# Kernel tuning notes

Hardware: AMD Instinct MI355X
Metric: run time of the kernel (lower is better)

## Reference

```python
import jax, jax.numpy as jnp
import numpy as np

N = 50000        # nodes
DEG = 16         # in-degree per node
E = N * DEG      # edges
NF = 32          # node_feats
H = 4            # heads
EF = 32          # e_feats
SLOPE = 0.2      # negative_slope


def setup_inputs() -> dict:
    key = jax.random.key(0)
    ks = jax.random.split(key, 8)
    h = jax.random.normal(ks[0], (N, NF), dtype=jnp.float32)
    e = jax.random.normal(ks[1], (E, EF), dtype=jnp.float32)
    src = jax.random.randint(ks[2], (E,), 0, N)
    # every node has exactly DEG incoming edges (sorted by dst)
    dst = jnp.repeat(jnp.arange(N), DEG)
    W_node = jax.random.normal(ks[3], (NF, H * NF), dtype=jnp.float32) * 0.1
    W_edge = jax.random.normal(ks[4], (EF, H * NF), dtype=jnp.float32) * 0.1
    w_att = jax.random.normal(ks[5], (H, 3 * NF), dtype=jnp.float32) * 0.1
    W_scale = jax.random.normal(ks[6], (H * NF, NF), dtype=jnp.float32) * 0.1
    bias = jnp.zeros((NF,), dtype=jnp.float32)
    return {"h": h, "e": e, "src": src, "dst": dst, "W_node": W_node,
            "W_edge": W_edge, "w_att": w_att, "W_scale": W_scale, "bias": bias}


def reference(h, e, src, dst, W_node, W_edge, w_att, W_scale, bias):
    wv = (h @ W_node).reshape(N, H, NF)       # [N,H,F]
    we = (e @ W_edge).reshape(E, H, NF)       # [E,H,F]
    u = wv[src]                               # [E,H,F] src features per edge
    v = wv[dst]                               # [E,H,F] dst features per edge
    # attention = leaky_relu(<concat(u,e,v), w_att>) without materializing concat
    wa_u, wa_e, wa_v = jnp.split(w_att, 3, axis=-1)  # each [H,F]
    attn = (jnp.einsum('ehf,hf->eh', u, wa_u)
            + jnp.einsum('ehf,hf->eh', we, wa_e)
            + jnp.einsum('ehf,hf->eh', v, wa_v))
    attn = jax.nn.leaky_relu(attn, SLOPE)     # [E,H]
    # segment softmax over incoming edges of each dst node (stable)
    m = jax.lax.stop_gradient(jax.ops.segment_max(attn, dst, num_segments=N))
    ex = jnp.exp(attn - m[dst])
    denom = jax.ops.segment_sum(ex, dst, num_segments=N)
    score = ex / denom[dst]                   # [E,H]
    msg = score[:, :, None] * u * we          # [E,H,F]
    agg = jax.ops.segment_sum(msg, dst, num_segments=N).reshape(N, H * NF)
    return agg @ W_scale + bias               # [N,F]
```

## Files before the change

kernel.cpp:

```cpp
#include <hip/hip_runtime.h>
#include <math.h>

#define N_NODES 50000
#define DEG 16
#define NF 32
#define NHEAD 4
#define HF (NHEAD * NF)
#define EF 32
#define SLOPE 0.2f

__device__ __forceinline__ float bcastf(float v, int srclane) {
    return __uint_as_float((unsigned)__builtin_amdgcn_readlane((int)__float_as_uint(v), srclane));
}

__global__ __launch_bounds__(256) void k1_wv(
    const float* __restrict__ hfeat,
    const float* __restrict__ W_node,
    const float* __restrict__ w_att,
    float* __restrict__ wv,
    float* __restrict__ att_src,
    float* __restrict__ att_dst)
{
    const int wave = threadIdx.x >> 6;
    const int lane = threadIdx.x & 63;
    const int n = blockIdx.x * 4 + wave;
    const int j0 = 2 * lane;
    const int hh = lane >> 4;
    const int f0 = j0 & 31;

    float hv = hfeat[n * NF + (lane & 31)];
    float acc0 = 0.f, acc1 = 0.f;
#pragma unroll
    for (int k = 0; k < NF; ++k) {
        float hk = bcastf(hv, k);
        float2 wk = *reinterpret_cast<const float2*>(&W_node[k * HF + j0]);
        acc0 = fmaf(hk, wk.x, acc0);
        acc1 = fmaf(hk, wk.y, acc1);
    }
    *reinterpret_cast<float2*>(&wv[(size_t)n * HF + j0]) = make_float2(acc0, acc1);

    float2 wau = *reinterpret_cast<const float2*>(&w_att[hh * (3 * NF) + f0]);
    float2 wav = *reinterpret_cast<const float2*>(&w_att[hh * (3 * NF) + 2 * NF + f0]);
    float du = acc0 * wau.x + acc1 * wau.y;
    float dv = acc0 * wav.x + acc1 * wav.y;
#pragma unroll
    for (int m = 1; m < 16; m <<= 1) {
        du += __shfl_xor(du, m, 64);
        dv += __shfl_xor(dv, m, 64);
    }
    if ((lane & 15) == 0) {
        att_src[n * NHEAD + hh] = du;
        att_dst[n * NHEAD + hh] = dv;
    }
}

__global__ __launch_bounds__(256) void k2_main(
    const float* __restrict__ efeat,
    const int*   __restrict__ src,
    const float* __restrict__ W_edge,
    const float* __restrict__ w_att,
    const float* __restrict__ W_scale,
    const float* __restrict__ bias,
    const float* __restrict__ wv,
    const float* __restrict__ att_src,
    const float* __restrict__ att_dst,
    float* __restrict__ out)
{
    __shared__ float lds_agg[4][HF];

    const int wave = threadIdx.x >> 6;
    const int lane = threadIdx.x & 63;
    const int n = blockIdx.x * 4 + wave;
    const int j0 = 2 * lane;
    const int hh = lane >> 4;
    const int f0 = j0 & 31;

    float2 W[EF];
#pragma unroll
    for (int k = 0; k < EF; ++k)
        W[k] = *reinterpret_cast<const float2*>(&W_edge[k * HF + j0]);

    const float* eblk = efeat + (size_t)n * DEG * EF;
    float4 ea = *reinterpret_cast<const float4*>(eblk + lane * 8);
    float4 eb4 = *reinterpret_cast<const float4*>(eblk + lane * 8 + 4);
    float ebf[8] = {ea.x, ea.y, ea.z, ea.w, eb4.x, eb4.y, eb4.z, eb4.w};

    int sv = src[n * DEG + (lane & 15)];

    float2 wae = *reinterpret_cast<const float2*>(&w_att[hh * (3 * NF) + NF + f0]);
    float dvv = att_dst[n * NHEAD + hh];

    float m = -INFINITY, l = 0.f, acc0 = 0.f, acc1 = 0.f;

#pragma unroll
    for (int ed = 0; ed < DEG; ++ed) {
        const int s = __builtin_amdgcn_readlane(sv, ed);
        float2 uu = *reinterpret_cast<const float2*>(&wv[(size_t)s * HF + j0]);

        float we0 = 0.f, we1 = 0.f;
#pragma unroll
        for (int k = 0; k < EF; ++k) {
            const int idx = ed * EF + k;
            float ek = bcastf(ebf[idx & 7], idx >> 3);
            we0 = fmaf(ek, W[k].x, we0);
            we1 = fmaf(ek, W[k].y, we1);
        }
        float ap = we0 * wae.x + we1 * wae.y;
        ap += __shfl_xor(ap, 1, 64);
        ap += __shfl_xor(ap, 2, 64);
        ap += __shfl_xor(ap, 4, 64);
        ap += __shfl_xor(ap, 8, 64);
        float a = ap + att_src[(size_t)s * NHEAD + hh] + dvv;
        a = (a > 0.f) ? a : a * SLOPE;

        float mn = fmaxf(m, a);
        float corr = __expf(m - mn);
        float ex = __expf(a - mn);
        l = l * corr + ex;
        acc0 = acc0 * corr + ex * (uu.x * we0);
        acc1 = acc1 * corr + ex * (uu.y * we1);
        m = mn;
    }
    const float inv = 1.f / l;
    lds_agg[wave][j0] = acc0 * inv;
    lds_agg[wave][j0 + 1] = acc1 * inv;
    __syncthreads();

    const int c = lane & 31;
    const int half = lane >> 5;
    float part = 0.f;
#pragma unroll
    for (int jj = 0; jj < 64; ++jj) {
        const int j = half * 64 + jj;
        part = fmaf(lds_agg[wave][j], W_scale[j * NF + c], part);
    }
    part += __shfl_xor(part, 32, 64);
    if (lane < 32) out[(size_t)n * NF + lane] = part + bias[lane];
}

extern "C" void kernel_launch(void* const* d_in, const int* in_sizes, int n_in,
                              void* d_out, int out_size, void* d_ws, size_t ws_size,
                              hipStream_t stream) {
    const float* hfeat   = (const float*)d_in[0];
    const float* efeat   = (const float*)d_in[1];
    const int*   src     = (const int*)d_in[2];
    const float* W_node  = (const float*)d_in[4];
    const float* W_edge  = (const float*)d_in[5];
    const float* w_att   = (const float*)d_in[6];
    const float* W_scale = (const float*)d_in[7];
    const float* bias    = (const float*)d_in[8];
    float* out = (float*)d_out;

    float* wv      = (float*)d_ws;
    float* att_src = wv + (size_t)N_NODES * HF;
    float* att_dst = att_src + (size_t)N_NODES * NHEAD;

    dim3 block(256);
    dim3 grid(N_NODES / 4);
    k1_wv<<<grid, block, 0, stream>>>(hfeat, W_node, w_att, wv, att_src, att_dst);
    k2_main<<<grid, block, 0, stream>>>(efeat, src, W_edge, w_att, W_scale, bias,
                                        wv, att_src, att_dst, out);
}
```

Before: 352.7 us.

## Use wave-uniform scalar loads for edge/node features and reuse W_node across nodes

Both kernels drop the per-lane vector load followed by readlane broadcast. Edge features, node features and src indices are now read at wave-uniform addresses, so the compiler can emit scalar (SMEM) loads. k1 also keeps W_node in registers and processes five nodes per wave, amortizing the weight load. An empty asm barrier pins the weights in VGPRs. This trades VALU readlane work for scalar-cache loads, which may add latency or register pressure.

After: 398.0 us. 12.8% more time.

```diff
diff --git a/kernel.cpp b/kernel.cpp
--- a/kernel.cpp
+++ b/kernel.cpp
@@ -8,10 +8,7 @@
 #define HF (NHEAD * NF)
 #define EF 32
 #define SLOPE 0.2f
-
-__device__ __forceinline__ float bcastf(float v, int srclane) {
-    return __uint_as_float((unsigned)__builtin_amdgcn_readlane((int)__float_as_uint(v), srclane));
-}
+#define K1_NPW 5
 
 __global__ __launch_bounds__(256) void k1_wv(
     const float* __restrict__ hfeat,
@@ -21,36 +18,48 @@
     float* __restrict__ att_src,
     float* __restrict__ att_dst)
 {
-    const int wave = threadIdx.x >> 6;
+    const int wave = __builtin_amdgcn_readfirstlane(threadIdx.x >> 6);
     const int lane = threadIdx.x & 63;
-    const int n = blockIdx.x * 4 + wave;
     const int j0 = 2 * lane;
     const int hh = lane >> 4;
     const int f0 = j0 & 31;
 
-    float hv = hfeat[n * NF + (lane & 31)];
-    float acc0 = 0.f, acc1 = 0.f;
+    float2 W[NF];
 #pragma unroll
-    for (int k = 0; k < NF; ++k) {
-        float hk = bcastf(hv, k);
-        float2 wk = *reinterpret_cast<const float2*>(&W_node[k * HF + j0]);
-        acc0 = fmaf(hk, wk.x, acc0);
-        acc1 = fmaf(hk, wk.y, acc1);
-    }
-    *reinterpret_cast<float2*>(&wv[(size_t)n * HF + j0]) = make_float2(acc0, acc1);
+    for (int k = 0; k < NF; ++k)
+        W[k] = *reinterpret_cast<const float2*>(&W_node[k * HF + j0]);
+#pragma unroll
+    for (int k = 0; k < NF; ++k)
+        asm volatile("" : "+v"(W[k].x), "+v"(W[k].y));
 
-    float2 wau = *reinterpret_cast<const float2*>(&w_att[hh * (3 * NF) + f0]);
-    float2 wav = *reinterpret_cast<const float2*>(&w_att[hh * (3 * NF) + 2 * NF + f0]);
-    float du = acc0 * wau.x + acc1 * wau.y;
-    float dv = acc0 * wav.x + acc1 * wav.y;
+    const float2 wau = *reinterpret_cast<const float2*>(&w_att[hh * (3 * NF) + f0]);
+    const float2 wav = *reinterpret_cast<const float2*>(&w_att[hh * (3 * NF) + 2 * NF + f0]);
+
+    const int nbase = (blockIdx.x * 4 + wave) * K1_NPW;
 #pragma unroll
-    for (int m = 1; m < 16; m <<= 1) {
-        du += __shfl_xor(du, m, 64);
-        dv += __shfl_xor(dv, m, 64);
-    }
-    if ((lane & 15) == 0) {
-        att_src[n * NHEAD + hh] = du;
-        att_dst[n * NHEAD + hh] = dv;
+    for (int i = 0; i < K1_NPW; ++i) {
+        const int n = nbase + i;
+        const float* __restrict__ hrow = hfeat + (size_t)n * NF;
+        float acc0 = 0.f, acc1 = 0.f;
+#pragma unroll
+        for (int k = 0; k < NF; ++k) {
+            const float hk = hrow[k];
+            acc0 = fmaf(hk, W[k].x, acc0);
+            acc1 = fmaf(hk, W[k].y, acc1);
+        }
+        *reinterpret_cast<float2*>(&wv[(size_t)n * HF + j0]) = make_float2(acc0, acc1);
+
+        float du = acc0 * wau.x + acc1 * wau.y;
+        float dv = acc0 * wav.x + acc1 * wav.y;
+#pragma unroll
+        for (int m = 1; m < 16; m <<= 1) {
+            du += __shfl_xor(du, m, 64);
+            dv += __shfl_xor(dv, m, 64);
+        }
+        if ((lane & 15) == 0) {
+            att_src[n * NHEAD + hh] = du;
+            att_dst[n * NHEAD + hh] = dv;
+        }
     }
 }
 
@@ -68,7 +77,7 @@
 {
     __shared__ float lds_agg[4][HF];
 
-    const int wave = threadIdx.x >> 6;
+    const int wave = __builtin_amdgcn_readfirstlane(threadIdx.x >> 6);
     const int lane = threadIdx.x & 63;
     const int n = blockIdx.x * 4 + wave;
     const int j0 = 2 * lane;
@@ -79,29 +88,27 @@
 #pragma unroll
     for (int k = 0; k < EF; ++k)
         W[k] = *reinterpret_cast<const float2*>(&W_edge[k * HF + j0]);
+#pragma unroll
+    for (int k = 0; k < EF; ++k)
+        asm volatile("" : "+v"(W[k].x), "+v"(W[k].y));
 
-    const float* eblk = efeat + (size_t)n * DEG * EF;
-    float4 ea = *reinterpret_cast<const float4*>(eblk + lane * 8);
-    float4 eb4 = *reinterpret_cast<const float4*>(eblk + lane * 8 + 4);
-    float ebf[8] = {ea.x, ea.y, ea.z, ea.w, eb4.x, eb4.y, eb4.z, eb4.w};
+    const float* __restrict__ erow = efeat + (size_t)n * (DEG * EF);
+    const int*   __restrict__ srow = src + n * DEG;
 
-    int sv = src[n * DEG + (lane & 15)];
-
-    float2 wae = *reinterpret_cast<const float2*>(&w_att[hh * (3 * NF) + NF + f0]);
-    float dvv = att_dst[n * NHEAD + hh];
+    const float2 wae = *reinterpret_cast<const float2*>(&w_att[hh * (3 * NF) + NF + f0]);
+    const float dvv = att_dst[n * NHEAD + hh];
 
     float m = -INFINITY, l = 0.f, acc0 = 0.f, acc1 = 0.f;
 
 #pragma unroll
     for (int ed = 0; ed < DEG; ++ed) {
-        const int s = __builtin_amdgcn_readlane(sv, ed);
+        const int s = srow[ed];
         float2 uu = *reinterpret_cast<const float2*>(&wv[(size_t)s * HF + j0]);
 
         float we0 = 0.f, we1 = 0.f;
 #pragma unroll
         for (int k = 0; k < EF; ++k) {
-            const int idx = ed * EF + k;
-            float ek = bcastf(ebf[idx & 7], idx >> 3);
+            const float ek = erow[ed * EF + k];
             we0 = fmaf(ek, W[k].x, we0);
             we1 = fmaf(ek, W[k].y, we1);
         }
@@ -156,8 +163,8 @@
     float* att_dst = att_src + (size_t)N_NODES * NHEAD;
 
     dim3 block(256);
-    dim3 grid(N_NODES / 4);
-    k1_wv<<<grid, block, 0, stream>>>(hfeat, W_node, w_att, wv, att_src, att_dst);
-    k2_main<<<grid, block, 0, stream>>>(efeat, src, W_edge, w_att, W_scale, bias,
-                                        wv, att_src, att_dst, out);
+    k1_wv<<<dim3(N_NODES / (4 * K1_NPW)), block, 0, stream>>>(
+        hfeat, W_node, w_att, wv, att_src, att_dst);
+    k2_main<<<dim3(N_NODES / 4), block, 0, stream>>>(
+        efeat, src, W_edge, w_att, W_scale, bias, wv, att_src, att_dst, out);
 }
```

## Reuse W_node columns in registers across 16 nodes per block in k1

Applied to the files above, without the earlier changes.

k1 now has each thread own one output column, keep that column of W_node in registers, and loop over 16 nodes per block, reading h rows as broadcast float4 loads. This replaces the per-node reload of W_node and the readlane broadcasts. k2 gets an occupancy hint of 4 in its launch bounds and an empty asm barrier that pins the W_edge registers so they are not rematerialized. The trade-offs are a smaller k1 grid and extra register pressure in k2.

New measurement: 337.8 us. 4.2% less time.

```diff
diff --git a/kernel.cpp b/kernel.cpp
--- a/kernel.cpp
+++ b/kernel.cpp
@@ -8,12 +8,13 @@
 #define HF (NHEAD * NF)
 #define EF 32
 #define SLOPE 0.2f
+#define K1_NPB 16
 
 __device__ __forceinline__ float bcastf(float v, int srclane) {
     return __uint_as_float((unsigned)__builtin_amdgcn_readlane((int)__float_as_uint(v), srclane));
 }
 
-__global__ __launch_bounds__(256) void k1_wv(
+__global__ __launch_bounds__(256, 4) void k1_wv(
     const float* __restrict__ hfeat,
     const float* __restrict__ W_node,
     const float* __restrict__ w_att,
@@ -21,40 +22,50 @@
     float* __restrict__ att_src,
     float* __restrict__ att_dst)
 {
-    const int wave = threadIdx.x >> 6;
-    const int lane = threadIdx.x & 63;
-    const int n = blockIdx.x * 4 + wave;
-    const int j0 = 2 * lane;
-    const int hh = lane >> 4;
-    const int f0 = j0 & 31;
+    const int t = threadIdx.x;
+    const int half = t >> 7;
+    const int j = t & 127;
+    const int hh = j >> 5;
+    const int f = j & 31;
 
-    float hv = hfeat[n * NF + (lane & 31)];
-    float acc0 = 0.f, acc1 = 0.f;
+    float Wn[NF];
 #pragma unroll
-    for (int k = 0; k < NF; ++k) {
-        float hk = bcastf(hv, k);
-        float2 wk = *reinterpret_cast<const float2*>(&W_node[k * HF + j0]);
-        acc0 = fmaf(hk, wk.x, acc0);
-        acc1 = fmaf(hk, wk.y, acc1);
-    }
-    *reinterpret_cast<float2*>(&wv[(size_t)n * HF + j0]) = make_float2(acc0, acc1);
+    for (int k = 0; k < NF; ++k)
+        Wn[k] = W_node[k * HF + j];
 
-    float2 wau = *reinterpret_cast<const float2*>(&w_att[hh * (3 * NF) + f0]);
-    float2 wav = *reinterpret_cast<const float2*>(&w_att[hh * (3 * NF) + 2 * NF + f0]);
-    float du = acc0 * wau.x + acc1 * wau.y;
-    float dv = acc0 * wav.x + acc1 * wav.y;
+    const float wu  = w_att[hh * (3 * NF) + f];
+    const float wvv = w_att[hh * (3 * NF) + 2 * NF + f];
+
 #pragma unroll
-    for (int m = 1; m < 16; m <<= 1) {
-        du += __shfl_xor(du, m, 64);
-        dv += __shfl_xor(dv, m, 64);
-    }
-    if ((lane & 15) == 0) {
-        att_src[n * NHEAD + hh] = du;
-        att_dst[n * NHEAD + hh] = dv;
+    for (int i = 0; i < K1_NPB / 2; ++i) {
+        const int n = blockIdx.x * K1_NPB + i * 2 + half;
+        const float* __restrict__ hrow = hfeat + (size_t)n * NF;
+        float acc = 0.f;
+#pragma unroll
+        for (int k4 = 0; k4 < NF / 4; ++k4) {
+            const float4 h4 = *reinterpret_cast<const float4*>(hrow + k4 * 4);
+            acc = fmaf(h4.x, Wn[k4 * 4 + 0], acc);
+            acc = fmaf(h4.y, Wn[k4 * 4 + 1], acc);
+            acc = fmaf(h4.z, Wn[k4 * 4 + 2], acc);
+            acc = fmaf(h4.w, Wn[k4 * 4 + 3], acc);
+        }
+        wv[(size_t)n * HF + j] = acc;
+
+        float du = acc * wu;
+        float dv = acc * wvv;
+#pragma unroll
+        for (int mm = 1; mm < 32; mm <<= 1) {
+            du += __shfl_xor(du, mm, 64);
+            dv += __shfl_xor(dv, mm, 64);
+        }
+        if (f == 0) {
+            att_src[n * NHEAD + hh] = du;
+            att_dst[n * NHEAD + hh] = dv;
+        }
     }
 }
 
-__global__ __launch_bounds__(256) void k2_main(
+__global__ __launch_bounds__(256, 4) void k2_main(
     const float* __restrict__ efeat,
     const int*   __restrict__ src,
     const float* __restrict__ W_edge,
@@ -79,16 +90,19 @@
 #pragma unroll
     for (int k = 0; k < EF; ++k)
         W[k] = *reinterpret_cast<const float2*>(&W_edge[k * HF + j0]);
+#pragma unroll
+    for (int k = 0; k < EF; ++k)
+        asm volatile("" : "+v"(W[k].x), "+v"(W[k].y));
 
     const float* eblk = efeat + (size_t)n * DEG * EF;
-    float4 ea = *reinterpret_cast<const float4*>(eblk + lane * 8);
+    float4 ea  = *reinterpret_cast<const float4*>(eblk + lane * 8);
     float4 eb4 = *reinterpret_cast<const float4*>(eblk + lane * 8 + 4);
     float ebf[8] = {ea.x, ea.y, ea.z, ea.w, eb4.x, eb4.y, eb4.z, eb4.w};
 
     int sv = src[n * DEG + (lane & 15)];
 
-    float2 wae = *reinterpret_cast<const float2*>(&w_att[hh * (3 * NF) + NF + f0]);
-    float dvv = att_dst[n * NHEAD + hh];
+    const float2 wae = *reinterpret_cast<const float2*>(&w_att[hh * (3 * NF) + NF + f0]);
+    const float dvv = att_dst[n * NHEAD + hh];
 
     float m = -INFINITY, l = 0.f, acc0 = 0.f, acc1 = 0.f;
 
@@ -156,8 +170,8 @@
     float* att_dst = att_src + (size_t)N_NODES * NHEAD;
 
     dim3 block(256);
-    dim3 grid(N_NODES / 4);
-    k1_wv<<<grid, block, 0, stream>>>(hfeat, W_node, w_att, wv, att_src, att_dst);
-    k2_main<<<grid, block, 0, stream>>>(efeat, src, W_edge, w_att, W_scale, bias,
-                                        wv, att_src, att_dst, out);
+    k1_wv<<<dim3(N_NODES / K1_NPB), block, 0, stream>>>(
+        hfeat, W_node, w_att, wv, att_src, att_dst);
+    k2_main<<<dim3(N_NODES / 4), block, 0, stream>>>(
+        efeat, src, W_edge, w_att, W_scale, bias, wv, att_src, att_dst, out);
 }
```
